# Performance work log

Hardware: AMD Instinct MI355X
Metric: run time of the kernel (lower is better)

## Reference

```python
import jax, jax.numpy as jnp
import numpy as np

NEG_SLOPE = 0.2  # PyG GATConv default LeakyReLU slope


def _leaky_relu(x):
    return jnp.where(x >= 0, x, NEG_SLOPE * x)


def gat_conv(x, edge_index, W, a_src, a_dst, b, concat):
    """Faithful PyG GATConv: gather -> leakyrelu attention -> per-dst softmax -> scatter.
    x: [N, Fin], edge_index: [2, E] (src, dst), W: [Fin, H*C], a_src/a_dst: [H, C], b: [H*C] or [C].
    """
    N = x.shape[0]
    H, C = a_src.shape
    src, dst = edge_index[0], edge_index[1]
    h = (x @ W).reshape(N, H, C)                       # [N, H, C]
    alpha_s = jnp.einsum('nhc,hc->nh', h, a_src)       # [N, H]
    alpha_d = jnp.einsum('nhc,hc->nh', h, a_dst)       # [N, H]
    e = _leaky_relu(alpha_s[src] + alpha_d[dst])       # [E, H]
    # numerically stable softmax over edges grouped by destination node
    m = jax.ops.segment_max(e, dst, num_segments=N)    # [N, H]
    e = jnp.exp(e - m[dst])                            # [E, H]
    denom = jax.ops.segment_sum(e, dst, num_segments=N)  # [N, H]
    alpha = e / denom[dst]                             # [E, H]
    msg = h[src] * alpha[:, :, None]                   # [E, H, C]
    out = jax.ops.segment_sum(msg, dst, num_segments=N)  # [N, H, C]
    out = out.reshape(N, H * C) if concat else out.mean(axis=1)
    return out + b


def setup_inputs() -> dict:
    key = jax.random.key(0)
    ks = jax.random.split(key, 12)
    N, E, Fin, Fout = 100000, 1600000, 256, 40
    H1, C1 = 8, 8
    x = jax.random.normal(ks[0], (N, Fin), dtype=jnp.float32)
    edge_index = jax.random.randint(ks[1], (2, E), 0, N, dtype=jnp.int64)
    g = lambda k, shape: jax.random.normal(k, shape, dtype=jnp.float32) * np.float32(np.sqrt(2.0 / (shape[0] + shape[-1])))
    return {
        'x': x,
        'edge_index': edge_index,
        'W1': g(ks[2], (Fin, H1 * C1)),
        'a1_src': g(ks[3], (H1, C1)),
        'a1_dst': g(ks[4], (H1, C1)),
        'b1': jnp.zeros((H1 * C1,), dtype=jnp.float32),
        'W2': g(ks[5], (H1 * C1, Fout)),
        'a2_src': g(ks[6], (1, Fout)),
        'a2_dst': g(ks[7], (1, Fout)),
        'b2': jnp.zeros((Fout,), dtype=jnp.float32),
    }


def reference(x, edge_index, W1, a1_src, a1_dst, b1, W2, a2_src, a2_dst, b2):
    N = x.shape[0]
    # PyG GATConv adds self-loops by default
    loops = jnp.arange(N, dtype=edge_index.dtype)
    ei = jnp.concatenate([edge_index, jnp.stack([loops, loops])], axis=1)
    h = gat_conv(x, ei, W1, a1_src, a1_dst, b1, concat=True)   # [N, 64]
    h = jax.nn.relu(h)  # F.dropout is identity in eval mode
    h = gat_conv(h, ei, W2, a2_src, a2_dst, b2, concat=False)  # [N, Fout]
    return jax.nn.log_softmax(h, axis=1)
```

## Files before the change

### kernel.cpp

```cpp
#include <hip/hip_runtime.h>
#include <math.h>

#define NEG_SLOPE 0.2f
__device__ __forceinline__ float lrelu(float x){ return x >= 0.f ? x : NEG_SLOPE * x; }

typedef __attribute__((ext_vector_type(8))) short bf16x8;
typedef __attribute__((ext_vector_type(4))) float f32x4;

__device__ __forceinline__ float wred_sum(float v){
  #pragma unroll
  for (int o = 32; o; o >>= 1) v += __shfl_xor(v, o, 64);
  return v;
}

__device__ __forceinline__ float bfhi_f(float f){
  return __uint_as_float(__float_as_uint(f) & 0xFFFF0000u);
}
__device__ __forceinline__ unsigned short f2bf(float f){
  unsigned u = __float_as_uint(f);
  unsigned r = u + 0x7FFFu + ((u >> 16) & 1u);
  return (unsigned short)(r >> 16);
}

__global__ __launch_bounds__(256) void k_bincnt(const int* __restrict__ ei, int E, int N, int nb,
                                                unsigned* __restrict__ bcnt){
  __shared__ unsigned h[512];
  const int tot = E + N;
  for (int i = threadIdx.x; i < nb; i += 256) h[i] = 0;
  __syncthreads();
  int base = blockIdx.x * 8192;
  #pragma unroll 4
  for (int j = 0; j < 32; j++){
    int e = base + threadIdx.x + j * 256;
    if (e < tot){
      unsigned d = (e < E) ? (unsigned)ei[E + e] : (unsigned)(e - E);
      atomicAdd(&h[d >> 8], 1u);
    }
  }
  __syncthreads();
  for (int i = threadIdx.x; i < nb; i += 256)
    if (h[i]) atomicAdd(&bcnt[i], h[i]);
}

__global__ void k_bscan(const unsigned* __restrict__ bcnt, unsigned* __restrict__ bbase,
                        unsigned* __restrict__ bcur, int nb, int tot){
  __shared__ unsigned s[512];
  int t = threadIdx.x;
  unsigned v = (t < nb) ? bcnt[t] : 0u;
  s[t] = v; __syncthreads();
  for (int off = 1; off < 512; off <<= 1){
    unsigned x = (t >= off) ? s[t - off] : 0u; __syncthreads();
    s[t] += x; __syncthreads();
  }
  if (t < nb){ unsigned b = s[t] - v; bbase[t] = b; bcur[t] = b; }
  if (t == 0) bbase[nb] = (unsigned)tot;
}

__global__ __launch_bounds__(256) void k_binscat(const int* __restrict__ ei, int E, int N, int nb,
    unsigned* __restrict__ bcur, unsigned* __restrict__ staged){
  __shared__ unsigned sd[8192];
  __shared__ unsigned hist[512];
  __shared__ unsigned runb[512];
  const int tot = E + N;
  for (int i = threadIdx.x; i < nb; i += 256) hist[i] = 0;
  __syncthreads();
  int base = blockIdx.x * 8192;
  #pragma unroll 4
  for (int j = 0; j < 32; j++){
    int idx = threadIdx.x + j * 256;
    int e = base + idx;
    unsigned d = 0xFFFFFFFFu;
    if (e < tot) d = (e < E) ? (unsigned)ei[E + e] : (unsigned)(e - E);
    sd[idx] = d;
    if (d != 0xFFFFFFFFu) atomicAdd(&hist[d >> 8], 1u);
  }
  __syncthreads();
  for (int i = threadIdx.x; i < nb; i += 256){
    unsigned c = hist[i];
    runb[i] = c ? atomicAdd(&bcur[i], c) : 0u;
    hist[i] = 0;
  }
  __syncthreads();
  #pragma unroll 4
  for (int j = 0; j < 32; j++){
    int idx = threadIdx.x + j * 256;
    unsigned d = sd[idx];
    if (d == 0xFFFFFFFFu) continue;
    int e = base + idx;
    unsigned s = (e < E) ? (unsigned)ei[e] : d;
    unsigned b = d >> 8;
    unsigned pos = runb[b] + atomicAdd(&hist[b], 1u);
    staged[pos] = s | ((d & 255u) << 20);
  }
}

__global__ __launch_bounds__(256) void k_csr(const unsigned* __restrict__ bbase,
    const unsigned* __restrict__ staged, int N,
    unsigned* __restrict__ off_, unsigned* __restrict__ cur, int* __restrict__ srcids){
  __shared__ unsigned cnt[256], scn[256], cnt2[256];
  int b = blockIdx.x, t = threadIdx.x;
  unsigned beg = bbase[b], end = bbase[b + 1];
  cnt[t] = 0; cnt2[t] = 0;
  __syncthreads();
  for (unsigned i = beg + t; i < end; i += 256)
    atomicAdd(&cnt[staged[i] >> 20], 1u);
  __syncthreads();
  unsigned v = cnt[t];
  scn[t] = v; __syncthreads();
  for (int off = 1; off < 256; off <<= 1){
    unsigned x = (t >= off) ? scn[t - off] : 0u; __syncthreads();
    scn[t] += x; __syncthreads();
  }
  unsigned ex = scn[t] - v;
  int d = b * 256 + t;
  if (d < N){ off_[d] = beg + ex; cur[d] = beg + ex + v; }
  cnt[t] = ex;
  __syncthreads();
  for (unsigned i = beg + t; i < end; i += 256){
    unsigned u = staged[i];
    unsigned dl = u >> 20;
    unsigned pos = beg + cnt[dl] + atomicAdd(&cnt2[dl], 1u);
    srcids[pos] = (int)(u & 0xFFFFFu);
  }
}

__global__ void k_wprep(const float* __restrict__ W, short* __restrict__ wt_hi,
                        short* __restrict__ wt_lo){
  int i = blockIdx.x * 256 + threadIdx.x;
  int k = i >> 6, c = i & 63;
  float v = W[i];
  unsigned u = __float_as_uint(v);
  wt_hi[c * 256 + k] = (short)(u >> 16);
  float lo = v - bfhi_f(v);
  wt_lo[c * 256 + k] = (short)(__float_as_uint(lo) >> 16);
}

__global__ void k_w2prep(const float* __restrict__ W2, short* __restrict__ hi,
                         short* __restrict__ lo){
  int i = blockIdx.x * 256 + threadIdx.x;
  if (i >= 48 * 64) return;
  int c = i >> 6, k = i & 63;
  float v = (c < 40) ? W2[k * 40 + c] : 0.f;
  unsigned u = __float_as_uint(v);
  hi[c * 64 + k] = (short)(u >> 16);
  float l = v - bfhi_f(v);
  lo[c * 64 + k] = (short)(__float_as_uint(l) >> 16);
}

__global__ __launch_bounds__(256) void k_gemm1_mfma(const float* __restrict__ x,
    const unsigned* __restrict__ wtu_hi, const unsigned* __restrict__ wtu_lo,
    const float* __restrict__ a1s, const float* __restrict__ a1d,
    unsigned short* __restrict__ h1b, float* __restrict__ as_, float* __restrict__ ad_, int N){
  __shared__ unsigned ldsB[2][64 * 132];
  int lane = threadIdx.x & 63;
  int wv   = threadIdx.x >> 6;
  int r0   = blockIdx.x * 64 + wv * 16;
  int col16 = lane & 15;
  int kg    = lane >> 4;

  #pragma unroll
  for (int j = 0; j < 32; j++){
    int g = threadIdx.x + j * 256;
    int row = g >> 7, col = g & 127;
    ldsB[0][row * 132 + col] = wtu_hi[g];
    ldsB[1][row * 132 + col] = wtu_lo[g];
  }
  __syncthreads();
  if (r0 >= N) return;

  const float* xr = x + (size_t)min(r0 + col16, N - 1) * 256 + kg * 8;

  f32x4 acc[4];
  #pragma unroll
  for (int ct = 0; ct < 4; ct++) acc[ct] = (f32x4){0.f, 0.f, 0.f, 0.f};

  #pragma unroll 2
  for (int kt = 0; kt < 8; kt++){
    float4 v0 = *(const float4*)(xr + kt * 32);
    float4 v1 = *(const float4*)(xr + kt * 32 + 4);
    unsigned u[8] = {__float_as_uint(v0.x), __float_as_uint(v0.y), __float_as_uint(v0.z), __float_as_uint(v0.w),
                     __float_as_uint(v1.x), __float_as_uint(v1.y), __float_as_uint(v1.z), __float_as_uint(v1.w)};
    union { bf16x8 v; unsigned u[4]; } ahi, alo;
    #pragma unroll
    for (int j = 0; j < 4; j++)
      ahi.u[j] = __builtin_amdgcn_perm(u[2*j+1], u[2*j], 0x07060302);
    float lo[8];
    lo[0] = v0.x - bfhi_f(v0.x); lo[1] = v0.y - bfhi_f(v0.y);
    lo[2] = v0.z - bfhi_f(v0.z); lo[3] = v0.w - bfhi_f(v0.w);
    lo[4] = v1.x - bfhi_f(v1.x); lo[5] = v1.y - bfhi_f(v1.y);
    lo[6] = v1.z - bfhi_f(v1.z); lo[7] = v1.w - bfhi_f(v1.w);
    #pragma unroll
    for (int j = 0; j < 4; j++)
      alo.u[j] = __builtin_amdgcn_perm(__float_as_uint(lo[2*j+1]), __float_as_uint(lo[2*j]), 0x07060302);

    #pragma unroll
    for (int ct = 0; ct < 4; ct++){
      int wcol = ct * 16 + col16;
      const bf16x8 bhi = *(const bf16x8*)(&ldsB[0][wcol * 132 + kt * 16 + kg * 4]);
      const bf16x8 blo = *(const bf16x8*)(&ldsB[1][wcol * 132 + kt * 16 + kg * 4]);
      acc[ct] = __builtin_amdgcn_mfma_f32_16x16x32_bf16(ahi.v, bhi, acc[ct], 0, 0, 0);
      acc[ct] = __builtin_amdgcn_mfma_f32_16x16x32_bf16(ahi.v, blo, acc[ct], 0, 0, 0);
      acc[ct] = __builtin_amdgcn_mfma_f32_16x16x32_bf16(alo.v, bhi, acc[ct], 0, 0, 0);
    }
  }

  float cs[4], cd[4];
  #pragma unroll
  for (int ct = 0; ct < 4; ct++){ cs[ct] = a1s[ct * 16 + col16]; cd[ct] = a1d[ct * 16 + col16]; }
  #pragma unroll
  for (int r = 0; r < 4; r++){
    int rr = r0 + kg * 4 + r;
    bool ok = rr < N;
    #pragma unroll
    for (int ct = 0; ct < 4; ct++){
      float v = acc[ct][r];
      if (ok) h1b[(size_t)rr * 64 + ct * 16 + col16] = f2bf(v);
      float s = v * cs[ct];
      float t = v * cd[ct];
      s += __shfl_xor(s, 1, 64); s += __shfl_xor(s, 2, 64); s += __shfl_xor(s, 4, 64);
      t += __shfl_xor(t, 1, 64); t += __shfl_xor(t, 2, 64); t += __shfl_xor(t, 4, 64);
      if (ok && (col16 & 7) == 0){
        int head = ct * 2 + (col16 >> 3);
        as_[(size_t)rr * 8 + head] = s;
        ad_[(size_t)rr * 8 + head] = t;
      }
    }
  }
}

__global__ __launch_bounds__(256) void k_gat1(const unsigned* __restrict__ off_, const unsigned* __restrict__ cur,
    const int* __restrict__ srcids, const float* __restrict__ as_, const float* __restrict__ ad_,
    const unsigned short* __restrict__ h1b, const float* __restrict__ b1,
    unsigned short* __restrict__ out1b, int N){
  int lane = threadIdx.x & 63;
  int wv   = threadIdx.x >> 6;
  int d    = blockIdx.x * 4 + wv;
  if (d >= N) return;
  __shared__ float lds_p[4][64 * 8];
  __shared__ int   lds_s[4][64];
  float* lp = lds_p[wv];
  int*   ls = lds_s[wv];
  unsigned beg = off_[d], fin = cur[d];

  int e8 = lane >> 3, h = lane & 7;
  int c0 = lane & 31, pe = lane >> 5, hh = c0 >> 2;
  float adh = ad_[(size_t)d * 8 + h];
  float psacc = 0.f, accx = 0.f, accy = 0.f;

  for (unsigned base = beg; base < fin; base += 64){
    int nthis = (int)min(64u, fin - base);
    unsigned i = base + lane;
    ls[lane] = (i < fin) ? srcids[i] : 0;
    asm volatile("s_waitcnt lgkmcnt(0)" ::: "memory");
    __builtin_amdgcn_sched_barrier(0);
    for (int j = 0; j < nthis; j += 8){
      int eloc = j + e8;
      int s = ls[eloc];
      float p = 0.f;
      if (eloc < nthis) p = __expf(lrelu(as_[(size_t)s * 8 + h] + adh));
      lp[eloc * 8 + h] = p;
      psacc += p;
    }
    asm volatile("s_waitcnt lgkmcnt(0)" ::: "memory");
    __builtin_amdgcn_sched_barrier(0);
    for (int e = 0; e < nthis; e += 8){
      int e0 = e + pe, e1 = e + 2 + pe, e2 = e + 4 + pe, e3 = e + 6 + pe;
      float p0 = lp[e0 * 8 + hh], p1 = lp[e1 * 8 + hh];
      float p2 = lp[e2 * 8 + hh], p3 = lp[e3 * 8 + hh];
      int s0 = ls[e0], s1 = ls[e1], s2 = ls[e2], s3 = ls[e3];
      unsigned u0 = *(const unsigned*)(h1b + (size_t)s0 * 64 + c0 * 2);
      unsigned u1 = *(const unsigned*)(h1b + (size_t)s1 * 64 + c0 * 2);
      unsigned u2 = *(const unsigned*)(h1b + (size_t)s2 * 64 + c0 * 2);
      unsigned u3 = *(const unsigned*)(h1b + (size_t)s3 * 64 + c0 * 2);
      accx = fmaf(p0, __uint_as_float(u0 << 16), accx);
      accy = fmaf(p0, __uint_as_float(u0 & 0xFFFF0000u), accy);
      accx = fmaf(p1, __uint_as_float(u1 << 16), accx);
      accy = fmaf(p1, __uint_as_float(u1 & 0xFFFF0000u), accy);
      accx = fmaf(p2, __uint_as_float(u2 << 16), accx);
      accy = fmaf(p2, __uint_as_float(u2 & 0xFFFF0000u), accy);
      accx = fmaf(p3, __uint_as_float(u3 << 16), accx);
      accy = fmaf(p3, __uint_as_float(u3 & 0xFFFF0000u), accy);
    }
    asm volatile("" ::: "memory");
  }
  float den = psacc;
  den += __shfl_xor(den, 8, 64);
  den += __shfl_xor(den, 16, 64);
  den += __shfl_xor(den, 32, 64);
  float mydenv = __shfl(den, hh, 64);
  accx += __shfl_xor(accx, 32, 64);
  accy += __shfl_xor(accy, 32, 64);
  if (lane < 32){
    int ch = lane * 2;
    float v0 = accx / mydenv + b1[ch];
    float v1 = accy / mydenv + b1[ch + 1];
    ushort2 o;
    o.x = f2bf(v0 > 0.f ? v0 : 0.f);
    o.y = f2bf(v1 > 0.f ? v1 : 0.f);
    *(ushort2*)(out1b + (size_t)d * 64 + ch) = o;
  }
}

__global__ __launch_bounds__(256) void k_gemm2m(const unsigned short* __restrict__ out1b,
    const short* __restrict__ wt2_hi, const short* __restrict__ wt2_lo,
    const float* __restrict__ a2s, const float* __restrict__ a2d,
    unsigned short* __restrict__ h2b, float* __restrict__ as_, float* __restrict__ ad_, int N){
  int lane = threadIdx.x & 63;
  int wv   = threadIdx.x >> 6;
  int r0   = blockIdx.x * 64 + wv * 16;
  if (r0 >= N) return;
  int col16 = lane & 15;
  int kg    = lane >> 4;
  const unsigned short* ar = out1b + (size_t)min(r0 + col16, N - 1) * 64 + kg * 8;

  f32x4 acc[3];
  #pragma unroll
  for (int ct = 0; ct < 3; ct++) acc[ct] = (f32x4){0.f, 0.f, 0.f, 0.f};

  #pragma unroll
  for (int kt = 0; kt < 2; kt++){
    const bf16x8 a = *(const bf16x8*)(ar + kt * 32);
    #pragma unroll
    for (int ct = 0; ct < 3; ct++){
      int wcol = ct * 16 + col16;
      const bf16x8 bhi = *(const bf16x8*)(wt2_hi + wcol * 64 + kt * 32 + kg * 8);
      const bf16x8 blo = *(const bf16x8*)(wt2_lo + wcol * 64 + kt * 32 + kg * 8);
      acc[ct] = __builtin_amdgcn_mfma_f32_16x16x32_bf16(a, bhi, acc[ct], 0, 0, 0);
      acc[ct] = __builtin_amdgcn_mfma_f32_16x16x32_bf16(a, blo, acc[ct], 0, 0, 0);
    }
  }

  float cs[3], cd[3];
  #pragma unroll
  for (int ct = 0; ct < 3; ct++){
    int col = ct * 16 + col16;
    bool okc = col < 40;
    cs[ct] = okc ? a2s[col] : 0.f;
    cd[ct] = okc ? a2d[col] : 0.f;
  }
  #pragma unroll
  for (int r = 0; r < 4; r++){
    int rr = r0 + kg * 4 + r;
    bool ok = rr < N;
    float s = 0.f, t = 0.f;
    #pragma unroll
    for (int ct = 0; ct < 3; ct++){
      s = fmaf(acc[ct][r], cs[ct], s);
      t = fmaf(acc[ct][r], cd[ct], t);
      int col = ct * 16 + col16;
      if (ok && col < 40) h2b[(size_t)rr * 40 + col] = f2bf(acc[ct][r]);
    }
    s += __shfl_xor(s, 1, 64); s += __shfl_xor(s, 2, 64);
    s += __shfl_xor(s, 4, 64); s += __shfl_xor(s, 8, 64);
    t += __shfl_xor(t, 1, 64); t += __shfl_xor(t, 2, 64);
    t += __shfl_xor(t, 4, 64); t += __shfl_xor(t, 8, 64);
    if (ok && col16 == 0){ as_[rr] = s; ad_[rr] = t; }
  }
}

__global__ __launch_bounds__(256) void k_gat2(const unsigned* __restrict__ off_, const unsigned* __restrict__ cur,
    const int* __restrict__ srcids, const float* __restrict__ as_, const float* __restrict__ ad_,
    const unsigned short* __restrict__ h2b, const float* __restrict__ b2, float* __restrict__ out, int N){
  int lane = threadIdx.x & 63;
  int wv   = threadIdx.x >> 6;
  int d    = blockIdx.x * 4 + wv;
  if (d >= N) return;
  __shared__ float lds_p[4][64];
  __shared__ int   lds_s[4][64];
  float* lp = lds_p[wv];
  int*   ls = lds_s[wv];
  unsigned beg = off_[d], fin = cur[d];
  float add = ad_[d];

  int c0 = lane & 31;
  int pe = lane >> 5;
  int idx = c0 < 20 ? c0 : 19;
  float ps = 0.f, accx = 0.f, accy = 0.f;

  for (unsigned base = beg; base < fin; base += 64){
    unsigned i = base + lane;
    int nthis = (int)min(64u, fin - base);
    if (i < fin){
      int s = srcids[i];
      float p = __expf(lrelu(as_[s] + add));
      ps += p; ls[lane] = s; lp[lane] = p;
    } else { ls[lane] = 0; lp[lane] = 0.f; }
    asm volatile("s_waitcnt lgkmcnt(0)" ::: "memory");
    __builtin_amdgcn_sched_barrier(0);
    for (int e = 0; e < nthis; e += 8){
      int e0 = e + pe, e1 = e + 2 + pe, e2 = e + 4 + pe, e3 = e + 6 + pe;
      float p0 = lp[e0], p1 = lp[e1], p2 = lp[e2], p3 = lp[e3];
      int s0 = ls[e0], s1 = ls[e1], s2 = ls[e2], s3 = ls[e3];
      unsigned u0 = *(const unsigned*)(h2b + (size_t)s0 * 40 + idx * 2);
      unsigned u1 = *(const unsigned*)(h2b + (size_t)s1 * 40 + idx * 2);
      unsigned u2 = *(const unsigned*)(h2b + (size_t)s2 * 40 + idx * 2);
      unsigned u3 = *(const unsigned*)(h2b + (size_t)s3 * 40 + idx * 2);
      accx = fmaf(p0, __uint_as_float(u0 << 16), accx);
      accy = fmaf(p0, __uint_as_float(u0 & 0xFFFF0000u), accy);
      accx = fmaf(p1, __uint_as_float(u1 << 16), accx);
      accy = fmaf(p1, __uint_as_float(u1 & 0xFFFF0000u), accy);
      accx = fmaf(p2, __uint_as_float(u2 << 16), accx);
      accy = fmaf(p2, __uint_as_float(u2 & 0xFFFF0000u), accy);
      accx = fmaf(p3, __uint_as_float(u3 << 16), accx);
      accy = fmaf(p3, __uint_as_float(u3 & 0xFFFF0000u), accy);
    }
    asm volatile("" ::: "memory");
  }
  ps = wred_sum(ps);
  accx += __shfl_xor(accx, 32, 64);
  accy += __shfl_xor(accy, 32, 64);

  float v0 = accx / ps + b2[idx * 2];
  float v1 = accy / ps + b2[idx * 2 + 1];
  bool act = (c0 < 20);
  float mx = act ? fmaxf(v0, v1) : -INFINITY;
  #pragma unroll
  for (int o = 16; o; o >>= 1) mx = fmaxf(mx, __shfl_xor(mx, o, 64));
  float exs = act ? (__expf(v0 - mx) + __expf(v1 - mx)) : 0.f;
  #pragma unroll
  for (int o = 16; o; o >>= 1) exs += __shfl_xor(exs, o, 64);
  float lse = mx + logf(exs);
  if (lane < 20){
    float2 o2; o2.x = v0 - lse; o2.y = v1 - lse;
    *(float2*)(out + (size_t)d * 40 + lane * 2) = o2;
  }
}

extern "C" void kernel_launch(void* const* d_in, const int* in_sizes, int n_in,
                              void* d_out, int out_size, void* d_ws, size_t ws_size,
                              hipStream_t stream){
  const float* x   = (const float*)d_in[0];
  const int*   ei  = (const int*)d_in[1];
  const float* W1  = (const float*)d_in[2];
  const float* a1s = (const float*)d_in[3];
  const float* a1d = (const float*)d_in[4];
  const float* b1  = (const float*)d_in[5];
  const float* W2  = (const float*)d_in[6];
  const float* a2s = (const float*)d_in[7];
  const float* a2d = (const float*)d_in[8];
  const float* b2  = (const float*)d_in[9];
  float* out = (float*)d_out;

  const int N = in_sizes[0] / 256;
  const int E = in_sizes[1] / 2;
  const int tot = E + N;
  const int nb  = (N + 255) >> 8;

  float* ws = (float*)d_ws;
  size_t o = 0;
  float* as1  = ws + o; o += (size_t)N * 8;
  float* ad1  = ws + o; o += (size_t)N * 8;
  unsigned short* out1b = (unsigned short*)(ws + o); o += (size_t)N * 32;
  unsigned short* h1b   = (unsigned short*)(ws + o); o += (size_t)N * 32;
  unsigned short* h2b   = (unsigned short*)(ws + o); o += (size_t)N * 20;
  unsigned* off_ = (unsigned*)(ws + o); o += (size_t)N;
  unsigned* cur  = (unsigned*)(ws + o); o += (size_t)N;
  int* srcids    = (int*)(ws + o);      o += (size_t)tot;
  short* wt_hi   = (short*)(ws + o);    o += 8192;
  short* wt_lo   = (short*)(ws + o);    o += 8192;
  short* wt2_hi  = (short*)(ws + o);    o += 1536;
  short* wt2_lo  = (short*)(ws + o);    o += 1536;
  unsigned* bcnt  = (unsigned*)(ws + o); o += nb;
  unsigned* bbase = (unsigned*)(ws + o); o += nb + 1;
  unsigned* bcur  = (unsigned*)(ws + o); o += nb;
  unsigned* staged = (unsigned*)out1b;
  float* as2 = as1;
  float* ad2 = ad1;

  const int cb = (tot + 8191) / 8192;

  hipMemsetAsync(bcnt, 0, sizeof(unsigned) * (size_t)nb, stream);

  k_bincnt <<<cb, 256, 0, stream>>>(ei, E, N, nb, bcnt);
  k_bscan  <<<1, 512, 0, stream>>>(bcnt, bbase, bcur, nb, tot);
  k_binscat<<<cb, 256, 0, stream>>>(ei, E, N, nb, bcur, staged);
  k_csr    <<<nb, 256, 0, stream>>>(bbase, staged, N, off_, cur, srcids);

  k_wprep <<<64, 256, 0, stream>>>(W1, wt_hi, wt_lo);
  k_w2prep<<<12, 256, 0, stream>>>(W2, wt2_hi, wt2_lo);

  k_gemm1_mfma<<<(N + 63) / 64, 256, 0, stream>>>(x, (const unsigned*)wt_hi, (const unsigned*)wt_lo,
                                                  a1s, a1d, h1b, as1, ad1, N);
  k_gat1 <<<(N + 3) / 4, 256, 0, stream>>>(off_, cur, srcids, as1, ad1, h1b, b1, out1b, N);

  k_gemm2m<<<(N + 63) / 64, 256, 0, stream>>>(out1b, wt2_hi, wt2_lo, a2s, a2d, h2b, as2, ad2, N);
  k_gat2  <<<(N + 3) / 4, 256, 0, stream>>>(off_, cur, srcids, as2, ad2, h2b, b2, out, N);
}
```

Before: 234.8 us.

## Process two row tiles per wave and stage W1 in halves to shrink LDS

The first-layer MFMA GEMM now gives each wave two 16-row tiles (128 rows per block). This halves the number of blocks and reuses each LDS weight fragment for twice as many MFMAs. The W1 hi/lo weights are staged in two K halves through a 64x68 LDS buffer instead of the full 64x132, cutting LDS use per block and possibly raising occupancy. The cost is an extra barrier per half, twice the accumulator registers, and the old whole-block early exit is replaced by per-tile guards in the epilogue.

Result: no change. 234.1 us (-0.3%).

```diff
diff --git a/kernel.cpp b/kernel.cpp
--- a/kernel.cpp
+++ b/kernel.cpp
@@ -20,6 +20,24 @@
   unsigned u = __float_as_uint(f);
   unsigned r = u + 0x7FFFu + ((u >> 16) & 1u);
   return (unsigned short)(r >> 16);
+}
+
+__device__ __forceinline__ void cvt_hilo(float4 v0, float4 v1, bf16x8* hi, bf16x8* lo){
+  unsigned u[8] = {__float_as_uint(v0.x), __float_as_uint(v0.y), __float_as_uint(v0.z), __float_as_uint(v0.w),
+                   __float_as_uint(v1.x), __float_as_uint(v1.y), __float_as_uint(v1.z), __float_as_uint(v1.w)};
+  union { bf16x8 v; unsigned u[4]; } H, L;
+  #pragma unroll
+  for (int j = 0; j < 4; j++)
+    H.u[j] = __builtin_amdgcn_perm(u[2*j+1], u[2*j], 0x07060302);
+  float l[8];
+  l[0] = v0.x - bfhi_f(v0.x); l[1] = v0.y - bfhi_f(v0.y);
+  l[2] = v0.z - bfhi_f(v0.z); l[3] = v0.w - bfhi_f(v0.w);
+  l[4] = v1.x - bfhi_f(v1.x); l[5] = v1.y - bfhi_f(v1.y);
+  l[6] = v1.z - bfhi_f(v1.z); l[7] = v1.w - bfhi_f(v1.w);
+  #pragma unroll
+  for (int j = 0; j < 4; j++)
+    L.u[j] = __builtin_amdgcn_perm(__float_as_uint(l[2*j+1]), __float_as_uint(l[2*j]), 0x07060302);
+  *hi = H.v; *lo = L.v;
 }
 
 __global__ __launch_bounds__(256) void k_bincnt(const int* __restrict__ ei, int E, int N, int nb,
@@ -147,63 +165,9 @@
   lo[c * 64 + k] = (short)(__float_as_uint(l) >> 16);
 }
 
-__global__ __launch_bounds__(256) void k_gemm1_mfma(const float* __restrict__ x,
-    const unsigned* __restrict__ wtu_hi, const unsigned* __restrict__ wtu_lo,
+__device__ __forceinline__ void epi1(const f32x4* acc, int r0, int col16, int kg,
     const float* __restrict__ a1s, const float* __restrict__ a1d,
     unsigned short* __restrict__ h1b, float* __restrict__ as_, float* __restrict__ ad_, int N){
-  __shared__ unsigned ldsB[2][64 * 132];
-  int lane = threadIdx.x & 63;
-  int wv   = threadIdx.x >> 6;
-  int r0   = blockIdx.x * 64 + wv * 16;
-  int col16 = lane & 15;
-  int kg    = lane >> 4;
-
-  #pragma unroll
-  for (int j = 0; j < 32; j++){
-    int g = threadIdx.x + j * 256;
-    int row = g >> 7, col = g & 127;
-    ldsB[0][row * 132 + col] = wtu_hi[g];
-    ldsB[1][row * 132 + col] = wtu_lo[g];
-  }
-  __syncthreads();
-  if (r0 >= N) return;
-
-  const float* xr = x + (size_t)min(r0 + col16, N - 1) * 256 + kg * 8;
-
-  f32x4 acc[4];
-  #pragma unroll
-  for (int ct = 0; ct < 4; ct++) acc[ct] = (f32x4){0.f, 0.f, 0.f, 0.f};
-
-  #pragma unroll 2
-  for (int kt = 0; kt < 8; kt++){
-    float4 v0 = *(const float4*)(xr + kt * 32);
-    float4 v1 = *(const float4*)(xr + kt * 32 + 4);
-    unsigned u[8] = {__float_as_uint(v0.x), __float_as_uint(v0.y), __float_as_uint(v0.z), __float_as_uint(v0.w),
-                     __float_as_uint(v1.x), __float_as_uint(v1.y), __float_as_uint(v1.z), __float_as_uint(v1.w)};
-    union { bf16x8 v; unsigned u[4]; } ahi, alo;
-    #pragma unroll
-    for (int j = 0; j < 4; j++)
-      ahi.u[j] = __builtin_amdgcn_perm(u[2*j+1], u[2*j], 0x07060302);
-    float lo[8];
-    lo[0] = v0.x - bfhi_f(v0.x); lo[1] = v0.y - bfhi_f(v0.y);
-    lo[2] = v0.z - bfhi_f(v0.z); lo[3] = v0.w - bfhi_f(v0.w);
-    lo[4] = v1.x - bfhi_f(v1.x); lo[5] = v1.y - bfhi_f(v1.y);
-    lo[6] = v1.z - bfhi_f(v1.z); lo[7] = v1.w - bfhi_f(v1.w);
-    #pragma unroll
-    for (int j = 0; j < 4; j++)
-      alo.u[j] = __builtin_amdgcn_perm(__float_as_uint(lo[2*j+1]), __float_as_uint(lo[2*j]), 0x07060302);
-
-    #pragma unroll
-    for (int ct = 0; ct < 4; ct++){
-      int wcol = ct * 16 + col16;
-      const bf16x8 bhi = *(const bf16x8*)(&ldsB[0][wcol * 132 + kt * 16 + kg * 4]);
-      const bf16x8 blo = *(const bf16x8*)(&ldsB[1][wcol * 132 + kt * 16 + kg * 4]);
-      acc[ct] = __builtin_amdgcn_mfma_f32_16x16x32_bf16(ahi.v, bhi, acc[ct], 0, 0, 0);
-      acc[ct] = __builtin_amdgcn_mfma_f32_16x16x32_bf16(ahi.v, blo, acc[ct], 0, 0, 0);
-      acc[ct] = __builtin_amdgcn_mfma_f32_16x16x32_bf16(alo.v, bhi, acc[ct], 0, 0, 0);
-    }
-  }
-
   float cs[4], cd[4];
   #pragma unroll
   for (int ct = 0; ct < 4; ct++){ cs[ct] = a1s[ct * 16 + col16]; cd[ct] = a1d[ct * 16 + col16]; }
@@ -226,6 +190,66 @@
       }
     }
   }
+}
+
+__global__ __launch_bounds__(256) void k_gemm1_mfma(const float* __restrict__ x,
+    const unsigned* __restrict__ wtu_hi, const unsigned* __restrict__ wtu_lo,
+    const float* __restrict__ a1s, const float* __restrict__ a1d,
+    unsigned short* __restrict__ h1b, float* __restrict__ as_, float* __restrict__ ad_, int N){
+  __shared__ unsigned ldsB[2][64 * 68];
+  int lane = threadIdx.x & 63;
+  int wv   = threadIdx.x >> 6;
+  int col16 = lane & 15;
+  int kg    = lane >> 4;
+  int rA = blockIdx.x * 128 + wv * 16;
+  int rB = rA + 64;
+  const float* xA = x + (size_t)min(rA + col16, N - 1) * 256 + kg * 8;
+  const float* xB = x + (size_t)min(rB + col16, N - 1) * 256 + kg * 8;
+
+  f32x4 accA[4], accB[4];
+  #pragma unroll
+  for (int ct = 0; ct < 4; ct++){ accA[ct] = (f32x4){0.f,0.f,0.f,0.f}; accB[ct] = (f32x4){0.f,0.f,0.f,0.f}; }
+
+  #pragma unroll
+  for (int half = 0; half < 2; half++){
+    #pragma unroll
+    for (int j = 0; j < 16; j++){
+      int g = threadIdx.x + j * 256;
+      int row = g >> 6, col = g & 63;
+      ldsB[0][row * 68 + col] = wtu_hi[row * 128 + half * 64 + col];
+      ldsB[1][row * 68 + col] = wtu_lo[row * 128 + half * 64 + col];
+    }
+    __syncthreads();
+
+    #pragma unroll
+    for (int kt = 0; kt < 4; kt++){
+      int xo = half * 128 + kt * 32;
+      float4 a0 = *(const float4*)(xA + xo);
+      float4 a1v = *(const float4*)(xA + xo + 4);
+      float4 b0 = *(const float4*)(xB + xo);
+      float4 b1v = *(const float4*)(xB + xo + 4);
+      bf16x8 ahiA, aloA, ahiB, aloB;
+      cvt_hilo(a0, a1v, &ahiA, &aloA);
+      cvt_hilo(b0, b1v, &ahiB, &aloB);
+
+      #pragma unroll
+      for (int ct = 0; ct < 4; ct++){
+        int wcol = ct * 16 + col16;
+        const bf16x8 bhi = *(const bf16x8*)(&ldsB[0][wcol * 68 + kt * 16 + kg * 4]);
+        const bf16x8 blo = *(const bf16x8*)(&ldsB[1][wcol * 68 + kt * 16 + kg * 4]);
+        accA[ct] = __builtin_amdgcn_mfma_f32_16x16x32_bf16(ahiA, bhi, accA[ct], 0, 0, 0);
+        accA[ct] = __builtin_amdgcn_mfma_f32_16x16x32_bf16(ahiA, blo, accA[ct], 0, 0, 0);
+        accA[ct] = __builtin_amdgcn_mfma_f32_16x16x32_bf16(aloA, bhi, accA[ct], 0, 0, 0);
+        accB[ct] = __builtin_amdgcn_mfma_f32_16x16x32_bf16(ahiB, bhi, accB[ct], 0, 0, 0);
+        accB[ct] = __builtin_amdgcn_mfma_f32_16x16x32_bf16(ahiB, blo, accB[ct], 0, 0, 0);
+        accB[ct] = __builtin_amdgcn_mfma_f32_16x16x32_bf16(aloB, bhi, accB[ct], 0, 0, 0);
+      }
+    }
+    if (half == 0) __syncthreads();
+  }
+
+  if (rA < N) epi1(accA, rA, col16, kg, a1s, a1d, h1b, as_, ad_, N);
+  if (rB < N) epi1(accB, rB, col16, kg, a1s, a1d, h1b, as_, ad_, N);
 }
 
 __global__ __launch_bounds__(256) void k_gat1(const unsigned* __restrict__ off_, const unsigned* __restrict__ cur,
@@ -479,8 +503,8 @@
   k_wprep <<<64, 256, 0, stream>>>(W1, wt_hi, wt_lo);
   k_w2prep<<<12, 256, 0, stream>>>(W2, wt2_hi, wt2_lo);
 
-  k_gemm1_mfma<<<(N + 63) / 64, 256, 0, stream>>>(x, (const unsigned*)wt_hi, (const unsigned*)wt_lo,
-                                                  a1s, a1d, h1b, as1, ad1, N);
+  k_gemm1_mfma<<<(N + 127) / 128, 256, 0, stream>>>(x, (const unsigned*)wt_hi, (const unsigned*)wt_lo,
+                                                    a1s, a1d, h1b, as1, ad1, N);
   k_gat1 <<<(N + 3) / 4, 256, 0, stream>>>(off_, cur, srcids, as1, ad1, h1b, b1, out1b, N);
 
   k_gemm2m<<<(N + 63) / 64, 256, 0, stream>>>(out1b, wt2_hi, wt2_lo, a2s, a2d, h2b, as2, ad2, N);
```
